# Optimization experiments

Hardware: AMD Instinct MI355X
Metric: run time of the kernel (lower is better)

## Reference

```python
import jax, jax.numpy as jnp
import numpy as np

REG = 0.01  # cfg['mf']['reg']
NUM_USERS, NUM_ITEMS, H = 100000, 1000000, 64
B, K = 16384, 50


def setup_inputs() -> dict:
    key = jax.random.key(0)
    k1, k2, k3, k4, k5 = jax.random.split(key, 5)
    return {
        "user_weight": jax.random.normal(k1, (NUM_USERS, H), dtype=jnp.float32),
        "item_weight": jax.random.normal(k2, (NUM_ITEMS, H), dtype=jnp.float32),
        "user_bias": jnp.zeros((NUM_USERS, 1), dtype=jnp.float32),
        "item_bias": jnp.zeros((NUM_ITEMS, 1), dtype=jnp.float32),
        "bias": jnp.zeros((1,), dtype=jnp.float32),
        "target": jax.random.uniform(k3, (B, K), dtype=jnp.float32),
        "user": jax.random.randint(k4, (B,), 0, NUM_USERS),
        "item": jax.random.randint(k5, (B, K), 0, NUM_ITEMS),
    }


def reference(user_weight, item_weight, user_bias, item_bias, bias, target, user, item):
    # user_embedding(u) = user_weight[u] + user_bias[u] (scalar bias broadcast over H)
    ue = user_weight[user] + user_bias[user]            # [B, H]
    ie = item_weight[item] + item_bias[item]            # [B, K, H]
    # per-user dot against its K items + global scalar bias (replaces Python loop)
    pred = jnp.einsum('bh,bkh->bk', ue, ie) + bias[0]   # [B, K]
    mse = jnp.mean((pred - target) ** 2)
    reg = REG * jnp.mean(jnp.linalg.norm(ue, axis=-1)) \
        + REG * jnp.mean(jnp.linalg.norm(ie.reshape(-1, ie.shape[-1]), axis=-1))
    loss = mse + reg
    # pack predictions and scalar loss into one array
    return jnp.concatenate([pred.ravel(), loss[None]])
```

## Files before the change

### kernel.cpp

```cpp
#include <hip/hip_runtime.h>

constexpr int NB = 16384;
constexpr int NK = 50;
constexpr int NH = 64;
constexpr float REG = 0.01f;
constexpr int G  = 4;
constexpr int NGRP = 13;

__global__ __launch_bounds__(256, 3) void mf_main(
    const float* __restrict__ user_weight,
    const float* __restrict__ item_weight,
    const float* __restrict__ user_bias,
    const float* __restrict__ item_bias,
    const float* __restrict__ gbias,
    const float* __restrict__ target,
    const int*   __restrict__ user,
    const int*   __restrict__ item,
    float* __restrict__ out,
    float* __restrict__ acc)
{
    const int tid  = threadIdx.x;
    const int wave = tid >> 6;
    const int lane = tid & 63;
    const int q    = lane >> 4;
    const int l16  = lane & 15;
    const bool active = (lane < NK);
    const int kcl  = active ? lane : (NK - 1);

    __shared__ __align__(16) float s_it[4][NK * NH];
    __shared__ __align__(16) float s_ue[4][NH];
    __shared__ float s_red[3][4];

    float* __restrict__ sit = s_it[wave];
    float* __restrict__ sue = s_ue[wave];

    const float gb = gbias[0];

    int b = (blockIdx.x * 4 + wave) * G;

    int   u    = user[b];
    int   kidx = item[b * NK + kcl];
    float ubv  = user_bias[u];
    float tgt  = target[b * NK + kcl];
    float ibv  = item_bias[kidx];
    float uev  = user_weight[(size_t)u * NH + lane] + ubv;

    float4 r[NGRP];
    #pragma unroll
    for (int gr = 0; gr < NGRP; ++gr) {
        const int k  = gr * 4 + q;
        const int kk = (k < NK) ? k : (NK - 1);
        const int it = __shfl(kidx, kk);
        r[gr] = *reinterpret_cast<const float4*>(item_weight + (size_t)it * NH + l16 * 4);
    }

    float mse_acc = 0.f, ien_acc = 0.f, uen_acc = 0.f;

    #pragma unroll
    for (int g = 0; g < G; ++g) {
        #pragma unroll
        for (int gr = 0; gr < NGRP; ++gr) {
            const int k  = gr * 4 + q;
            const int ks = (k < NK) ? k : (NK - 1);
            *reinterpret_cast<float4*>(sit + ks * NH + ((l16 ^ (ks & 15)) << 2)) = r[gr];
        }
        sue[lane] = uev;

        float us = uev * uev;
        #pragma unroll
        for (int off = 32; off > 0; off >>= 1) us += __shfl_down(us, off);
        if (lane == 0) uen_acc += sqrtf(us);

        const float ibv_c = ibv, tgt_c = tgt;

        if (g + 1 < G) {
            u    = user[b + 1];
            kidx = item[(b + 1) * NK + kcl];
            ubv  = user_bias[u];
            tgt  = target[(b + 1) * NK + kcl];
            ibv  = item_bias[kidx];
            uev  = user_weight[(size_t)u * NH + lane] + ubv;
            #pragma unroll
            for (int gr = 0; gr < NGRP; ++gr) {
                const int k  = gr * 4 + q;
                const int kk = (k < NK) ? k : (NK - 1);
                const int it = __shfl(kidx, kk);
                r[gr] = *reinterpret_cast<const float4*>(item_weight + (size_t)it * NH + l16 * 4);
            }
        }

        const int ksw = kcl & 15;
        const float* rowbase = sit + kcl * NH;
        float dot = 0.f, sq = 0.f;
        #pragma unroll
        for (int j = 0; j < 16; ++j) {
            const float4 iv = *reinterpret_cast<const float4*>(rowbase + ((j ^ ksw) << 2));
            const float4 uv = *reinterpret_cast<const float4*>(sue + (j << 2));
            const float iex = iv.x + ibv_c;
            const float iey = iv.y + ibv_c;
            const float iez = iv.z + ibv_c;
            const float iew = iv.w + ibv_c;
            dot += iex * uv.x + iey * uv.y + iez * uv.z + iew * uv.w;
            sq  += iex * iex  + iey * iey  + iez * iez  + iew * iew;
        }
        const float pred = dot + gb;
        if (active) {
            out[b * NK + lane] = pred;
            const float d = pred - tgt_c;
            mse_acc += d * d;
            ien_acc += sqrtf(sq);
        }
        b += 1;
    }

    #pragma unroll
    for (int off = 32; off > 0; off >>= 1) {
        mse_acc += __shfl_down(mse_acc, off);
        ien_acc += __shfl_down(ien_acc, off);
    }
    if (lane == 0) {
        s_red[0][wave] = mse_acc;
        s_red[1][wave] = uen_acc;
        s_red[2][wave] = ien_acc;
    }
    __syncthreads();
    if (tid == 0) {
        atomicAdd(&acc[0], s_red[0][0] + s_red[0][1] + s_red[0][2] + s_red[0][3]);
        atomicAdd(&acc[1], s_red[1][0] + s_red[1][1] + s_red[1][2] + s_red[1][3]);
        atomicAdd(&acc[2], s_red[2][0] + s_red[2][1] + s_red[2][2] + s_red[2][3]);
    }
}

__global__ void mf_finish(const float* __restrict__ acc, float* __restrict__ out)
{
    const float inv_bk = 1.0f / (float)(NB * NK);
    const float mse = acc[0] * inv_bk;
    const float loss = mse + REG * (acc[1] / (float)NB) + REG * (acc[2] * inv_bk);
    out[NB * NK] = loss;
}

extern "C" void kernel_launch(void* const* d_in, const int* in_sizes, int n_in,
                              void* d_out, int out_size, void* d_ws, size_t ws_size,
                              hipStream_t stream) {
    const float* user_weight = (const float*)d_in[0];
    const float* item_weight = (const float*)d_in[1];
    const float* user_bias   = (const float*)d_in[2];
    const float* item_bias   = (const float*)d_in[3];
    const float* gbias       = (const float*)d_in[4];
    const float* target      = (const float*)d_in[5];
    const int*   user        = (const int*)d_in[6];
    const int*   item        = (const int*)d_in[7];
    float* out = (float*)d_out;
    float* acc = (float*)d_ws;

    hipMemsetAsync(acc, 0, 3 * sizeof(float), stream);
    mf_main<<<NB / (4 * G), 256, 0, stream>>>(user_weight, item_weight, user_bias, item_bias,
                                              gbias, target, user, item, out, acc);
    mf_finish<<<1, 1, 0, stream>>>(acc, out);
}
```

Baseline: 370.9 us.

## Replace LDS transpose with DPP row reductions, one user per wave

```diff
diff --git a/kernel.cpp b/kernel.cpp
--- a/kernel.cpp
+++ b/kernel.cpp
@@ -4,10 +4,23 @@
 constexpr int NK = 50;
 constexpr int NH = 64;
 constexpr float REG = 0.01f;
-constexpr int G  = 4;
 constexpr int NGRP = 13;
 
-__global__ __launch_bounds__(256, 3) void mf_main(
+template<int CTRL>
+__device__ __forceinline__ float dpp_movf(float x) {
+    return __int_as_float(__builtin_amdgcn_update_dpp(
+        0, __float_as_int(x), CTRL, 0xF, 0xF, true));
+}
+
+__device__ __forceinline__ float row16_sum(float x) {
+    x += dpp_movf<0xB1>(x);
+    x += dpp_movf<0x4E>(x);
+    x += dpp_movf<0x124>(x);
+    x += dpp_movf<0x128>(x);
+    return x;
+}
+
+__global__ __launch_bounds__(256, 5) void mf_main(
     const float* __restrict__ user_weight,
     const float* __restrict__ item_weight,
     const float* __restrict__ user_bias,
@@ -27,23 +40,21 @@
     const bool active = (lane < NK);
     const int kcl  = active ? lane : (NK - 1);
 
-    __shared__ __align__(16) float s_it[4][NK * NH];
-    __shared__ __align__(16) float s_ue[4][NH];
     __shared__ float s_red[3][4];
 
-    float* __restrict__ sit = s_it[wave];
-    float* __restrict__ sue = s_ue[wave];
+    const int b = blockIdx.x * 4 + wave;
 
     const float gb = gbias[0];
 
-    int b = (blockIdx.x * 4 + wave) * G;
+    const int   u    = user[b];
+    const float ubv  = user_bias[u];
+    const int   kidx = item[b * NK + kcl];
+    const float tgt  = target[b * NK + kcl];
+    const float ibv  = item_bias[kidx];
 
-    int   u    = user[b];
-    int   kidx = item[b * NK + kcl];
-    float ubv  = user_bias[u];
-    float tgt  = target[b * NK + kcl];
-    float ibv  = item_bias[kidx];
-    float uev  = user_weight[(size_t)u * NH + lane] + ubv;
+    float4 uv = *reinterpret_cast<const float4*>(
+        user_weight + (size_t)u * NH + (l16 << 2));
+    uv.x += ubv; uv.y += ubv; uv.z += ubv; uv.w += ubv;
 
     float4 r[NGRP];
     #pragma unroll
@@ -51,66 +62,41 @@
         const int k  = gr * 4 + q;
         const int kk = (k < NK) ? k : (NK - 1);
         const int it = __shfl(kidx, kk);
-        r[gr] = *reinterpret_cast<const float4*>(item_weight + (size_t)it * NH + l16 * 4);
+        r[gr] = *reinterpret_cast<const float4*>(
+            item_weight + (size_t)it * NH + (l16 << 2));
     }
 
-    float mse_acc = 0.f, ien_acc = 0.f, uen_acc = 0.f;
+    float keep_dot = 0.f, keep_sq = 0.f;
+    #pragma unroll
+    for (int gr = 0; gr < NGRP; ++gr) {
+        const int k  = gr * 4 + q;
+        const int kk = (k < NK) ? k : (NK - 1);
+        const float ibk = __shfl(ibv, kk);
+        const float iex = r[gr].x + ibk;
+        const float iey = r[gr].y + ibk;
+        const float iez = r[gr].z + ibk;
+        const float iew = r[gr].w + ibk;
+        float pd = iex * uv.x + iey * uv.y + iez * uv.z + iew * uv.w;
+        float ps = iex * iex  + iey * iey  + iez * iez  + iew * iew;
+        pd = row16_sum(pd);
+        ps = row16_sum(ps);
+        if (l16 == gr) { keep_dot = pd; keep_sq = ps; }
+    }
 
-    #pragma unroll
-    for (int g = 0; g < G; ++g) {
-        #pragma unroll
-        for (int gr = 0; gr < NGRP; ++gr) {
-            const int k  = gr * 4 + q;
-            const int ks = (k < NK) ? k : (NK - 1);
-            *reinterpret_cast<float4*>(sit + ks * NH + ((l16 ^ (ks & 15)) << 2)) = r[gr];
-        }
-        sue[lane] = uev;
+    const int srcl = ((kcl & 3) << 4) + (kcl >> 2);
+    const float dot = __shfl(keep_dot, srcl);
+    const float sq  = __shfl(keep_sq,  srcl);
 
-        float us = uev * uev;
-        #pragma unroll
-        for (int off = 32; off > 0; off >>= 1) us += __shfl_down(us, off);
-        if (lane == 0) uen_acc += sqrtf(us);
+    float us = uv.x * uv.x + uv.y * uv.y + uv.z * uv.z + uv.w * uv.w;
+    us = row16_sum(us);
 
-        const float ibv_c = ibv, tgt_c = tgt;
-
-        if (g + 1 < G) {
-            u    = user[b + 1];
-            kidx = item[(b + 1) * NK + kcl];
-            ubv  = user_bias[u];
-            tgt  = target[(b + 1) * NK + kcl];
-            ibv  = item_bias[kidx];
-            uev  = user_weight[(size_t)u * NH + lane] + ubv;
-            #pragma unroll
-            for (int gr = 0; gr < NGRP; ++gr) {
-                const int k  = gr * 4 + q;
-                const int kk = (k < NK) ? k : (NK - 1);
-                const int it = __shfl(kidx, kk);
-                r[gr] = *reinterpret_cast<const float4*>(item_weight + (size_t)it * NH + l16 * 4);
-            }
-        }
-
-        const int ksw = kcl & 15;
-        const float* rowbase = sit + kcl * NH;
-        float dot = 0.f, sq = 0.f;
-        #pragma unroll
-        for (int j = 0; j < 16; ++j) {
-            const float4 iv = *reinterpret_cast<const float4*>(rowbase + ((j ^ ksw) << 2));
-            const float4 uv = *reinterpret_cast<const float4*>(sue + (j << 2));
-            const float iex = iv.x + ibv_c;
-            const float iey = iv.y + ibv_c;
-            const float iez = iv.z + ibv_c;
-            const float iew = iv.w + ibv_c;
-            dot += iex * uv.x + iey * uv.y + iez * uv.z + iew * uv.w;
-            sq  += iex * iex  + iey * iey  + iez * iez  + iew * iew;
-        }
-        const float pred = dot + gb;
-        if (active) {
-            out[b * NK + lane] = pred;
-            const float d = pred - tgt_c;
-            mse_acc += d * d;
-            ien_acc += sqrtf(sq);
-        }
-        b += 1;
+    float mse_acc = 0.f, ien_acc = 0.f;
+    const float pred = dot + gb;
+    if (active) {
+        out[b * NK + lane] = pred;
+        const float d = pred - tgt;
+        mse_acc = d * d;
+        ien_acc = sqrtf(sq);
     }
 
     #pragma unroll
@@ -120,7 +106,7 @@
     }
     if (lane == 0) {
         s_red[0][wave] = mse_acc;
-        s_red[1][wave] = uen_acc;
+        s_red[1][wave] = sqrtf(us);
         s_red[2][wave] = ien_acc;
     }
     __syncthreads();
@@ -154,7 +140,7 @@
     float* acc = (float*)d_ws;
 
     hipMemsetAsync(acc, 0, 3 * sizeof(float), stream);
-    mf_main<<<NB / (4 * G), 256, 0, stream>>>(user_weight, item_weight, user_bias, item_bias,
-                                              gbias, target, user, item, out, acc);
+    mf_main<<<NB / 4, 256, 0, stream>>>(user_weight, item_weight, user_bias, item_bias,
+                                        gbias, target, user, item, out, acc);
     mf_finish<<<1, 1, 0, stream>>>(acc, out);
 }
```

New measurement: 463.3 us. 1.25x slower.
